# Kernel optimization log

Hardware: AMD Instinct MI355X
Metric: run time of the kernel (lower is better)

## Reference

```python
import jax, jax.numpy as jnp
import numpy as np
from jax import lax

NEG = -1e30  # finite stand-in for -inf to keep gradients clean
BLANK = 0


def _ctc_loss(log_probs, targets, logits_lengths, targets_lengths):
    # log_probs: (B, T, V) log-softmaxed; targets: (B, S) int; lengths: (B,)
    B, T, V = log_probs.shape
    S = targets.shape[1]
    L = 2 * S + 1  # extended label length: blank-interleaved

    # extended label sequence: [blank, t0, blank, t1, ..., blank]
    ext = jnp.zeros((B, L), dtype=targets.dtype).at[:, 1::2].set(targets)

    # gather log-probs of extended labels per time step -> (B, T, L)
    lp_ext = jnp.take_along_axis(
        log_probs, jnp.broadcast_to(ext[:, None, :], (B, T, L)), axis=2
    )

    # skip transition (s-2 -> s) allowed where ext[s] != blank and ext[s] != ext[s-2]
    skip = jnp.concatenate(
        [jnp.zeros((B, 2), dtype=bool),
         (ext[:, 2:] != ext[:, :-2]) & (ext[:, 2:] != BLANK)],
        axis=1,
    )

    # alpha init at t=0
    alpha0 = jnp.full((B, L), NEG, dtype=log_probs.dtype)
    alpha0 = alpha0.at[:, 0].set(lp_ext[:, 0, 0])
    alpha0 = alpha0.at[:, 1].set(
        jnp.where(targets_lengths > 0, lp_ext[:, 0, 1], NEG))

    neg1 = jnp.full((B, 1), NEG, dtype=log_probs.dtype)
    neg2 = jnp.full((B, 2), NEG, dtype=log_probs.dtype)

    def step(alpha, inp):
        lp_t, t = inp  # lp_t: (B, L)
        a1 = jnp.concatenate([neg1, alpha[:, :-1]], axis=1)
        a2 = jnp.where(skip, jnp.concatenate([neg2, alpha[:, :-2]], axis=1), NEG)
        new = jnp.logaddexp(jnp.logaddexp(alpha, a1), a2) + lp_t
        # freeze alpha once past each sequence's length so final read is at t=len-1
        alpha = jnp.where((t < logits_lengths)[:, None], new, alpha)
        return alpha, None

    lp_tbl = jnp.transpose(lp_ext, (1, 0, 2))  # (T, B, L)
    alpha, _ = lax.scan(step, alpha0, (lp_tbl[1:], jnp.arange(1, T)))

    # final states: last blank (index 2*tl) and last label (index 2*tl-1)
    idx_blank = (2 * targets_lengths).astype(jnp.int32)
    idx_label = jnp.maximum(2 * targets_lengths - 1, 0).astype(jnp.int32)
    a_blank = jnp.take_along_axis(alpha, idx_blank[:, None], axis=1)[:, 0]
    a_label = jnp.take_along_axis(alpha, idx_label[:, None], axis=1)[:, 0]
    a_label = jnp.where(targets_lengths > 0, a_label, NEG)
    return -jnp.logaddexp(a_blank, a_label)  # (B,)


def setup_inputs() -> dict:
    key = jax.random.key(0)
    k1, k2, k3, k4 = jax.random.split(key, 4)
    B, T, V, S = 32, 1024, 512, 128
    logits = jax.random.normal(k1, (B, T, V), dtype=jnp.float32)
    targets = jax.random.randint(k2, (B, S), 1, V, dtype=jnp.int32)  # avoid blank=0
    logits_lengths = jax.random.randint(k3, (B,), T // 2, T + 1, dtype=jnp.int32)
    targets_lengths = jax.random.randint(k4, (B,), S // 2, S + 1, dtype=jnp.int32)
    return {
        "logits": logits,
        "targets": targets,
        "logits_lengths": logits_lengths,
        "targets_lengths": targets_lengths,
    }


def reference(logits, targets, logits_lengths, targets_lengths):
    # after_logsoftmax=False -> apply log_softmax; time_major=False -> no permute
    log_probs = jax.nn.log_softmax(logits, axis=2)
    # reduce=None -> per-batch loss of shape (B,)
    return _ctc_loss(log_probs, targets, logits_lengths, targets_lengths)
```

## Files before the change

kernel.cpp:

```cpp
#include <hip/hip_runtime.h>

enum { B_ = 32, T_ = 1024, V_ = 512, S_ = 128 };

static constexpr float K2   = 1.4426950408889634f;
static constexpr float LN2F = 0.6931471805599453f;
#define BOOSTI 6

typedef float f32x4 __attribute__((ext_vector_type(4)));
#define AS1 __attribute__((address_space(1)))
#define AS3 __attribute__((address_space(3)))

#define DPPI(x, ctrl) __builtin_amdgcn_update_dpp(0, (x), (ctrl), 0xF, 0xF, true)
#define DPPF(x, ctrl) __int_as_float(DPPI(__float_as_int(x), (ctrl)))
#define DPP_WSR1(x) DPPF((x), 0x138)

__device__ __forceinline__ float dpp_wave_max_l63(float x) {
  x = fmaxf(x, DPPF(x, 0xB1));   x = fmaxf(x, DPPF(x, 0x4E));
  x = fmaxf(x, DPPF(x, 0x124));  x = fmaxf(x, DPPF(x, 0x128));
  x = fmaxf(x, DPPF(x, 0x142));  x = fmaxf(x, DPPF(x, 0x143));
  return x;
}

__global__ __launch_bounds__(256) void ctc_pre4(
    const float* __restrict__ logits, const int* __restrict__ targets,
    const int* __restrict__ tgtlen, f32x4* __restrict__ Q) {
  const int w = threadIdx.x >> 6, l = threadIdx.x & 63;
  const int row = blockIdx.x * 4 + w;
  const int b = row >> 10;
  const float* lrow = logits + (size_t)row * V_;
  const float4* r4 = (const float4*)lrow;
  float4 a = r4[l], c = r4[l + 64];
  float s = __builtin_exp2f(a.x * K2) + __builtin_exp2f(a.y * K2) +
            __builtin_exp2f(a.z * K2) + __builtin_exp2f(a.w * K2) +
            __builtin_exp2f(c.x * K2) + __builtin_exp2f(c.y * K2) +
            __builtin_exp2f(c.z * K2) + __builtin_exp2f(c.w * K2);
  #pragma unroll
  for (int off = 32; off; off >>= 1) s += __shfl_xor(s, off, 64);
  const float sh = (float)BOOSTI - __builtin_log2f(s);

  const int2 ee = ((const int2*)(targets + b * S_))[l];
  const int tl = tgtlen[b];
  const float lgb = __shfl(a.x, 0, 64);
  const float lg1 = lrow[ee.x];
  const float lg3 = lrow[ee.y];
  const float pb  = __builtin_exp2f(fmaf(lgb, K2, sh));
  const float pe1 = __builtin_exp2f(fmaf(lg1, K2, sh));
  const float pe3 = __builtin_exp2f(fmaf(lg3, K2, sh));
  const int smax = 2 * tl;
  f32x4 q;
  q.x = (4 * l + 1 <= smax) ? pe1 : 0.0f;
  q.y = (4 * l + 3 <= smax) ? pe3 : 0.0f;
  q.z = (4 * l     <= smax) ? pb  : 0.0f;
  q.w = (4 * l + 2 <= smax) ? pb  : 0.0f;
  Q[(size_t)row * 64 + l] = q;
}

__global__ __launch_bounds__(128, 1) void ctc_dp7(
    const f32x4* __restrict__ Q, const int* __restrict__ targets,
    const int* __restrict__ loglen, const int* __restrict__ tgtlen,
    float* __restrict__ out) {
  __shared__ f32x4 buf[2][32 * 64];
  __shared__ int flag_ready[2];
  __shared__ int flag_done[2];
  __shared__ float A[257];
  const int wv = threadIdx.x >> 6, l = threadIdx.x & 63;
  const int b = blockIdx.x;
  const int len = loglen[b], tl = tgtlen[b];
  const int nch = (len - 1 + 31) >> 5;
  const f32x4* Qb = Q + (size_t)b * T_ * 64;

  if (threadIdx.x == 0) {
    flag_ready[0] = 0; flag_ready[1] = 0;
    flag_done[0] = 0;  flag_done[1] = 0;
  }
  __syncthreads();

  if (wv == 1) {
    for (int c = 0; c < nch; ++c) {
      if (c >= 2) {
        while (((volatile int*)flag_done)[c & 1] < c - 1)
          __builtin_amdgcn_s_sleep(1);
      }
      const int r0 = 1 + 32 * c;
      #pragma unroll
      for (int i = 0; i < 32; ++i) {
        int row = r0 + i; if (row > T_ - 1) row = T_ - 1;
        __builtin_amdgcn_global_load_lds(
            (const AS1 void*)(const void*)(Qb + (size_t)row * 64 + l),
            (AS3 void*)(void*)(&buf[c & 1][i * 64]), 16, 0, 0);
      }
      asm volatile("s_waitcnt vmcnt(0)" ::: "memory");
      if (l == 0) ((volatile int*)flag_ready)[c & 1] = c + 1;
    }
    return;
  }

  const int2 ee = ((const int2*)(targets + b * S_))[l];
  const int e1 = ee.x, e3 = ee.y;
  const int em1 = __shfl_up(e3, 1);
  const float m1 = ((l > 0) && (e1 != 0) && (e1 != em1)) ? 1.0f : 0.0f;
  const float m3 = ((e3 != 0) && (e3 != e1)) ? 1.0f : 0.0f;
  const float v4l = ((l == 63) && (2 * tl >= 256)) ? 1.0f : 0.0f;

  f32x4 qi = Qb[l];
  float p0 = (l == 0) ? qi.z : 0.0f;
  float p1 = (l == 0) ? qi.x : 0.0f;
  float p2 = 0.0f, p3 = 0.0f, p4 = 0.0f;

  const unsigned bufbase = (unsigned)(uintptr_t)(AS3 char*)(void*)&buf[0][0];

  f32x4 q0, q1, q2, q3, q4, q5, q6, q7;
#define DSRO(R, O) asm volatile("ds_read_b128 %0, %1 offset:" #O \
      : "=&v"(R) : "v"(vb))
#define WTL(R, N) asm volatile("s_waitcnt lgkmcnt(" #N ")" : "+v"(R))

#define COMPUTE(RX) { \
    const float n1_  = DPP_WSR1(p3); \
    const float w0_ = (p0 + n1_) * RX.z; \
    const float w1_ = (p0 + p1 + n1_ * m1) * RX.x; \
    const float w2_ = (p1 + p2) * RX.w; \
    const float w3_ = (p2 + p3 + p1 * m3) * RX.y; \
    const float w4_ = (p4 + p3) * RX.w * v4l; \
    p0 = w0_; p1 = w1_; p2 = w2_; p3 = w3_; p4 = w4_; \
  }

#define RENORM { \
    float m_ = fmaxf(fmaxf(fmaxf(p0, p1), fmaxf(p2, p3)), p4); \
    m_ = dpp_wave_max_l63(m_); \
    const int wm_ = __builtin_amdgcn_readlane(__float_as_int(m_), 63); \
    const int e_ = (wm_ >> 23) & 0xFF; \
    const float sc_ = __int_as_float((254 - e_) << 23); \
    p0 *= sc_; p1 *= sc_; p2 *= sc_; p3 *= sc_; p4 *= sc_; \
    shift += e_ - 127; \
  }

#define FS(R, O)  { WTL(R, 7); COMPUTE(R); DSRO(R, O); }
#define FD(R, N)  { WTL(R, N); COMPUTE(R); }
#define TS(R, O, i)  { WTL(R, 7); if (t0 + (i) < len) COMPUTE(R); DSRO(R, O); }
#define TD(R, N, i)  { WTL(R, N); if (t0 + (i) < len) COMPUTE(R); }

  int shift = 0;
  for (int c = 0; c < nch; ++c) {
    const int t0 = 1 + 32 * c;
    while (((volatile int*)flag_ready)[c & 1] < c + 1)
      __builtin_amdgcn_s_sleep(1);
    const unsigned vb = bufbase + (unsigned)(c & 1) * 32768u + (unsigned)l * 16u;

    DSRO(q0, 0);    DSRO(q1, 1024); DSRO(q2, 2048); DSRO(q3, 3072);
    DSRO(q4, 4096); DSRO(q5, 5120); DSRO(q6, 6144); DSRO(q7, 7168);

    if (t0 + 31 < len) {
      FS(q0, 8192)  FS(q1, 9216)  FS(q2, 10240) FS(q3, 11264)
      FS(q4, 12288) FS(q5, 13312) FS(q6, 14336) FS(q7, 15360)
      FS(q0, 16384) FS(q1, 17408) FS(q2, 18432) FS(q3, 19456)
      FS(q4, 20480) FS(q5, 21504) FS(q6, 22528) FS(q7, 23552)
      RENORM
      FS(q0, 24576) FS(q1, 25600) FS(q2, 26624) FS(q3, 27648)
      FS(q4, 28672) FS(q5, 29696) FS(q6, 30720) FS(q7, 31744)
      FD(q0, 7) FD(q1, 6) FD(q2, 5) FD(q3, 4)
      FD(q4, 3) FD(q5, 2) FD(q6, 1) FD(q7, 0)
      RENORM
    } else {
      TS(q0, 8192, 0)   TS(q1, 9216, 1)   TS(q2, 10240, 2)  TS(q3, 11264, 3)
      TS(q4, 12288, 4)  TS(q5, 13312, 5)  TS(q6, 14336, 6)  TS(q7, 15360, 7)
      TS(q0, 16384, 8)  TS(q1, 17408, 9)  TS(q2, 18432, 10) TS(q3, 19456, 11)
      TS(q4, 20480, 12) TS(q5, 21504, 13) TS(q6, 22528, 14) TS(q7, 23552, 15)
      TS(q0, 24576, 16) TS(q1, 25600, 17) TS(q2, 26624, 18) TS(q3, 27648, 19)
      TS(q4, 28672, 20) TS(q5, 29696, 21) TS(q6, 30720, 22) TS(q7, 31744, 23)
      TD(q0, 7, 24) TD(q1, 6, 25) TD(q2, 5, 26) TD(q3, 4, 27)
      TD(q4, 3, 28) TD(q5, 2, 29) TD(q6, 1, 30) TD(q7, 0, 31)
    }

    asm volatile("s_waitcnt lgkmcnt(0)" ::: "memory");
    if (l == 0) ((volatile int*)flag_done)[c & 1] = c + 1;
  }

  A[4 * l + 0] = p0; A[4 * l + 1] = p1;
  A[4 * l + 2] = p2; A[4 * l + 3] = p3;
  if (l == 63) A[256] = p4;
  asm volatile("s_waitcnt lgkmcnt(0)" ::: "memory");
  if (l == 0) {
    const int ib = 2 * tl;
    const int il = (ib - 1) > 0 ? ib - 1 : 0;
    const float ab = A[ib];
    const float al = (tl > 0) ? A[il] : 0.0f;
    out[b] = -(__builtin_log2f(ab + al) + (float)(shift - BOOSTI * len)) * LN2F;
  }
}

extern "C" void kernel_launch(void* const* d_in, const int* in_sizes, int n_in,
                              void* d_out, int out_size, void* d_ws, size_t ws_size,
                              hipStream_t stream) {
  const float* logits  = (const float*)d_in[0];
  const int*   targets = (const int*)d_in[1];
  const int*   loglen  = (const int*)d_in[2];
  const int*   tgtlen  = (const int*)d_in[3];
  float* out = (float*)d_out;
  f32x4* Q = (f32x4*)d_ws;

  ctc_pre4<<<(B_ * T_) / 4, 256, 0, stream>>>(logits, targets, tgtlen, Q);
  ctc_dp7<<<B_, 128, 0, stream>>>(Q, targets, loglen, tgtlen, out);
}
```

Before: 66.35 us.

## Fuse log-softmax gather into DP kernel with three producer waves

Drops the separate preprocessing kernel and its workspace round-trip. Inside the single per-batch block, three producer wavefronts each compute the log-softmax normalisation and emission probabilities for every third 32-row chunk and write them to a triple-buffered LDS ring, while one consumer wave runs the alpha recursion. The consumer's LDS waits are also batched four reads at a time. The cost is that only 32 blocks now read the full logits tensor, so softmax throughput is bounded by three waves per CU and may not keep pace with the serial recursion.

Result: slower. 125.8 us (+89.6%).

```diff
diff --git a/kernel.cpp b/kernel.cpp
--- a/kernel.cpp
+++ b/kernel.cpp
@@ -7,7 +7,6 @@
 #define BOOSTI 6
 
 typedef float f32x4 __attribute__((ext_vector_type(4)));
-#define AS1 __attribute__((address_space(1)))
 #define AS3 __attribute__((address_space(3)))
 
 #define DPPI(x, ctrl) __builtin_amdgcn_update_dpp(0, (x), (ctrl), 0xF, 0xF, true)
@@ -20,102 +19,129 @@
   x = fmaxf(x, DPPF(x, 0x142));  x = fmaxf(x, DPPF(x, 0x143));
   return x;
 }
-
-__global__ __launch_bounds__(256) void ctc_pre4(
+#define DPP_SUM63(x) { \
+  x += DPPF(x, 0xB1);  x += DPPF(x, 0x4E);  x += DPPF(x, 0x124); \
+  x += DPPF(x, 0x128); x += DPPF(x, 0x142); x += DPPF(x, 0x143); }
+
+__global__ __launch_bounds__(256, 1) void ctc_fused(
     const float* __restrict__ logits, const int* __restrict__ targets,
-    const int* __restrict__ tgtlen, f32x4* __restrict__ Q) {
-  const int w = threadIdx.x >> 6, l = threadIdx.x & 63;
-  const int row = blockIdx.x * 4 + w;
-  const int b = row >> 10;
-  const float* lrow = logits + (size_t)row * V_;
-  const float4* r4 = (const float4*)lrow;
-  float4 a = r4[l], c = r4[l + 64];
-  float s = __builtin_exp2f(a.x * K2) + __builtin_exp2f(a.y * K2) +
-            __builtin_exp2f(a.z * K2) + __builtin_exp2f(a.w * K2) +
-            __builtin_exp2f(c.x * K2) + __builtin_exp2f(c.y * K2) +
-            __builtin_exp2f(c.z * K2) + __builtin_exp2f(c.w * K2);
-  #pragma unroll
-  for (int off = 32; off; off >>= 1) s += __shfl_xor(s, off, 64);
-  const float sh = (float)BOOSTI - __builtin_log2f(s);
-
-  const int2 ee = ((const int2*)(targets + b * S_))[l];
-  const int tl = tgtlen[b];
-  const float lgb = __shfl(a.x, 0, 64);
-  const float lg1 = lrow[ee.x];
-  const float lg3 = lrow[ee.y];
-  const float pb  = __builtin_exp2f(fmaf(lgb, K2, sh));
-  const float pe1 = __builtin_exp2f(fmaf(lg1, K2, sh));
-  const float pe3 = __builtin_exp2f(fmaf(lg3, K2, sh));
-  const int smax = 2 * tl;
-  f32x4 q;
-  q.x = (4 * l + 1 <= smax) ? pe1 : 0.0f;
-  q.y = (4 * l + 3 <= smax) ? pe3 : 0.0f;
-  q.z = (4 * l     <= smax) ? pb  : 0.0f;
-  q.w = (4 * l + 2 <= smax) ? pb  : 0.0f;
-  Q[(size_t)row * 64 + l] = q;
-}
-
-__global__ __launch_bounds__(128, 1) void ctc_dp7(
-    const f32x4* __restrict__ Q, const int* __restrict__ targets,
     const int* __restrict__ loglen, const int* __restrict__ tgtlen,
     float* __restrict__ out) {
-  __shared__ f32x4 buf[2][32 * 64];
-  __shared__ int flag_ready[2];
-  __shared__ int flag_done[2];
+  __shared__ f32x4 buf[3][32 * 64];
+  __shared__ int flag_ready[3], flag_done[3];
   __shared__ float A[257];
   const int wv = threadIdx.x >> 6, l = threadIdx.x & 63;
   const int b = blockIdx.x;
   const int len = loglen[b], tl = tgtlen[b];
   const int nch = (len - 1 + 31) >> 5;
-  const f32x4* Qb = Q + (size_t)b * T_ * 64;
+  const float* Lb = logits + (size_t)b * T_ * V_;
+
+  const int2 ee = ((const int2*)(targets + b * S_))[l];
+  const int e1 = ee.x, e3 = ee.y;
+  const int smax = 2 * tl;
 
   if (threadIdx.x == 0) {
-    flag_ready[0] = 0; flag_ready[1] = 0;
-    flag_done[0] = 0;  flag_done[1] = 0;
+    flag_ready[0] = flag_ready[1] = flag_ready[2] = 0;
+    flag_done[0] = flag_done[1] = flag_done[2] = 0;
   }
   __syncthreads();
 
-  if (wv == 1) {
-    for (int c = 0; c < nch; ++c) {
-      if (c >= 2) {
-        while (((volatile int*)flag_done)[c & 1] < c - 1)
+  if (wv != 0) {
+    const bool v0m = (4 * l     <= smax);
+    const bool v1m = (4 * l + 1 <= smax);
+    const bool v2m = (4 * l + 2 <= smax);
+    const bool v3m = (4 * l + 3 <= smax);
+    const int l16 = l * 16, e1b = e1 * 4, e3b = e3 * 4;
+
+    f32x4 pa0, pa1, pa2, pa3, pc0, pc1, pc2, pc3;
+    float g10, g11, g12, g13, g30, g31, g32, g33;
+
+#define PISS(s, ROW) { \
+    int rr_ = (ROW) > 1023 ? 1023 : (ROW); int rb_ = rr_ * 2048; \
+    asm volatile("global_load_dwordx4 %0, %1, %2" : "=&v"(pa##s) : "v"(rb_ + l16), "s"(Lb)); \
+    asm volatile("global_load_dwordx4 %0, %1, %2" : "=&v"(pc##s) : "v"(rb_ + 1024 + l16), "s"(Lb)); \
+    asm volatile("global_load_dword %0, %1, %2"   : "=&v"(g1##s) : "v"(rb_ + e1b), "s"(Lb)); \
+    asm volatile("global_load_dword %0, %1, %2"   : "=&v"(g3##s) : "v"(rb_ + e3b), "s"(Lb)); }
+
+#define PROW(i, s, VM, DO) { \
+    asm volatile("s_waitcnt vmcnt(" #VM ")" \
+        : "+v"(pa##s), "+v"(pc##s), "+v"(g1##s), "+v"(g3##s)); \
+    float x8_ = __builtin_exp2f(pa##s.x * K2) + __builtin_exp2f(pa##s.y * K2) + \
+                __builtin_exp2f(pa##s.z * K2) + __builtin_exp2f(pa##s.w * K2) + \
+                __builtin_exp2f(pc##s.x * K2) + __builtin_exp2f(pc##s.y * K2) + \
+                __builtin_exp2f(pc##s.z * K2) + __builtin_exp2f(pc##s.w * K2); \
+    DPP_SUM63(x8_); \
+    const float ss_ = __int_as_float(__builtin_amdgcn_readlane(__float_as_int(x8_), 63)); \
+    const float sh_ = (float)BOOSTI - __builtin_log2f(ss_); \
+    const float lgb_ = __int_as_float(__builtin_amdgcn_readfirstlane(__float_as_int(pa##s.x))); \
+    const float pe1_ = __builtin_exp2f(fmaf(g1##s, K2, sh_)); \
+    const float pe3_ = __builtin_exp2f(fmaf(g3##s, K2, sh_)); \
+    const float pb_  = __builtin_exp2f(fmaf(lgb_, K2, sh_)); \
+    f32x4 qq_; \
+    qq_.x = v1m ? pe1_ : 0.0f; qq_.y = v3m ? pe3_ : 0.0f; \
+    qq_.z = v0m ? pb_  : 0.0f; qq_.w = v2m ? pb_  : 0.0f; \
+    pbuf[(i) * 64 + l] = qq_; \
+    if (DO) { PISS(s, r0 + (i) + 4) } }
+
+#define PDRAIN asm volatile("s_waitcnt lgkmcnt(0)" ::: "memory");
+
+    for (int c = wv - 1; c < nch; c += 3) {
+      if (c >= 3) {
+        while (((volatile int*)flag_done)[c % 3] < c - 2)
           __builtin_amdgcn_s_sleep(1);
       }
       const int r0 = 1 + 32 * c;
-      #pragma unroll
-      for (int i = 0; i < 32; ++i) {
-        int row = r0 + i; if (row > T_ - 1) row = T_ - 1;
-        __builtin_amdgcn_global_load_lds(
-            (const AS1 void*)(const void*)(Qb + (size_t)row * 64 + l),
-            (AS3 void*)(void*)(&buf[c & 1][i * 64]), 16, 0, 0);
-      }
-      asm volatile("s_waitcnt vmcnt(0)" ::: "memory");
-      if (l == 0) ((volatile int*)flag_ready)[c & 1] = c + 1;
+      f32x4* pbuf = &buf[c % 3][0];
+      PISS(0, r0) PISS(1, r0 + 1) PISS(2, r0 + 2) PISS(3, r0 + 3)
+      PROW(0, 0, 12, 1)  PROW(1, 1, 12, 1)  PROW(2, 2, 12, 1)  PROW(3, 3, 12, 1)
+      PROW(4, 0, 12, 1)  PROW(5, 1, 12, 1)  PROW(6, 2, 12, 1)  PROW(7, 3, 12, 1)
+      PDRAIN
+      PROW(8, 0, 12, 1)  PROW(9, 1, 12, 1)  PROW(10, 2, 12, 1) PROW(11, 3, 12, 1)
+      PROW(12, 0, 12, 1) PROW(13, 1, 12, 1) PROW(14, 2, 12, 1) PROW(15, 3, 12, 1)
+      PDRAIN
+      PROW(16, 0, 12, 1) PROW(17, 1, 12, 1) PROW(18, 2, 12, 1) PROW(19, 3, 12, 1)
+      PROW(20, 0, 12, 1) PROW(21, 1, 12, 1) PROW(22, 2, 12, 1) PROW(23, 3, 12, 1)
+      PDRAIN
+      PROW(24, 0, 12, 1) PROW(25, 1, 12, 1) PROW(26, 2, 12, 1) PROW(27, 3, 12, 1)
+      PROW(28, 0, 12, 0) PROW(29, 1, 8, 0)  PROW(30, 2, 4, 0)  PROW(31, 3, 0, 0)
+      PDRAIN
+      if (l == 0) ((volatile int*)flag_ready)[c % 3] = c + 1;
     }
     return;
   }
 
-  const int2 ee = ((const int2*)(targets + b * S_))[l];
-  const int e1 = ee.x, e3 = ee.y;
   const int em1 = __shfl_up(e3, 1);
   const float m1 = ((l > 0) && (e1 != 0) && (e1 != em1)) ? 1.0f : 0.0f;
   const float m3 = ((e3 != 0) && (e3 != e1)) ? 1.0f : 0.0f;
-  const float v4l = ((l == 63) && (2 * tl >= 256)) ? 1.0f : 0.0f;
-
-  f32x4 qi = Qb[l];
-  float p0 = (l == 0) ? qi.z : 0.0f;
-  float p1 = (l == 0) ? qi.x : 0.0f;
+  const float v4l = ((l == 63) && (smax >= 256)) ? 1.0f : 0.0f;
+
+  const f32x4* R0 = (const f32x4*)Lb;
+  f32x4 a0 = R0[l], c0 = R0[l + 64];
+  float s0 = __builtin_exp2f(a0.x * K2) + __builtin_exp2f(a0.y * K2) +
+             __builtin_exp2f(a0.z * K2) + __builtin_exp2f(a0.w * K2) +
+             __builtin_exp2f(c0.x * K2) + __builtin_exp2f(c0.y * K2) +
+             __builtin_exp2f(c0.z * K2) + __builtin_exp2f(c0.w * K2);
+  DPP_SUM63(s0);
+  const float ss0 = __int_as_float(__builtin_amdgcn_readlane(__float_as_int(s0), 63));
+  const float sh0 = (float)BOOSTI - __builtin_log2f(ss0);
+  const float lgb0 = __int_as_float(__builtin_amdgcn_readfirstlane(__float_as_int(a0.x)));
+  const float lg10 = Lb[targets[b * S_]];
+  float p0 = (l == 0) ? __builtin_exp2f(fmaf(lgb0, K2, sh0)) : 0.0f;
+  float p1 = (l == 0) ? __builtin_exp2f(fmaf(lg10, K2, sh0)) : 0.0f;
   float p2 = 0.0f, p3 = 0.0f, p4 = 0.0f;
 
   const unsigned bufbase = (unsigned)(uintptr_t)(AS3 char*)(void*)&buf[0][0];
+  asm volatile("s_waitcnt vmcnt(0) lgkmcnt(0)" ::: "memory");
 
   f32x4 q0, q1, q2, q3, q4, q5, q6, q7;
 #define DSRO(R, O) asm volatile("ds_read_b128 %0, %1 offset:" #O \
-      : "=&v"(R) : "v"(vb))
-#define WTL(R, N) asm volatile("s_waitcnt lgkmcnt(" #N ")" : "+v"(R))
+      : "=&v"(R) : "v"(vb));
+#define WT4(RA, RB, RC, RD, N) asm volatile("s_waitcnt lgkmcnt(" #N ")" \
+      : "+v"(RA), "+v"(RB), "+v"(RC), "+v"(RD));
+#define WTL(R, N) asm volatile("s_waitcnt lgkmcnt(" #N ")" : "+v"(R));
 
 #define COMPUTE(RX) { \
-    const float n1_  = DPP_WSR1(p3); \
+    const float n1_ = DPP_WSR1(p3); \
     const float w0_ = (p0 + n1_) * RX.z; \
     const float w1_ = (p0 + p1 + n1_ * m1) * RX.x; \
     const float w2_ = (p1 + p2) * RX.w; \
@@ -123,7 +149,6 @@
     const float w4_ = (p4 + p3) * RX.w * v4l; \
     p0 = w0_; p1 = w1_; p2 = w2_; p3 = w3_; p4 = w4_; \
   }
-
 #define RENORM { \
     float m_ = fmaxf(fmaxf(fmaxf(p0, p1), fmaxf(p2, p3)), p4); \
     m_ = dpp_wave_max_l63(m_); \
@@ -133,32 +158,30 @@
     p0 *= sc_; p1 *= sc_; p2 *= sc_; p3 *= sc_; p4 *= sc_; \
     shift += e_ - 127; \
   }
-
-#define FS(R, O)  { WTL(R, 7); COMPUTE(R); DSRO(R, O); }
-#define FD(R, N)  { WTL(R, N); COMPUTE(R); }
-#define TS(R, O, i)  { WTL(R, 7); if (t0 + (i) < len) COMPUTE(R); DSRO(R, O); }
-#define TD(R, N, i)  { WTL(R, N); if (t0 + (i) < len) COMPUTE(R); }
+#define CD(R, O) { COMPUTE(R); DSRO(R, O); }
+#define TS(R, O, i) { WTL(R, 7); if (t0 + (i) < len) COMPUTE(R); DSRO(R, O); }
+#define TD(R, N, i) { WTL(R, N); if (t0 + (i) < len) COMPUTE(R); }
 
   int shift = 0;
   for (int c = 0; c < nch; ++c) {
     const int t0 = 1 + 32 * c;
-    while (((volatile int*)flag_ready)[c & 1] < c + 1)
+    while (((volatile int*)flag_ready)[c % 3] < c + 1)
       __builtin_amdgcn_s_sleep(1);
-    const unsigned vb = bufbase + (unsigned)(c & 1) * 32768u + (unsigned)l * 16u;
-
-    DSRO(q0, 0);    DSRO(q1, 1024); DSRO(q2, 2048); DSRO(q3, 3072);
-    DSRO(q4, 4096); DSRO(q5, 5120); DSRO(q6, 6144); DSRO(q7, 7168);
+    const unsigned vb = bufbase + (unsigned)(c % 3) * 32768u + (unsigned)l * 16u;
+
+    DSRO(q0, 0)    DSRO(q1, 1024) DSRO(q2, 2048) DSRO(q3, 3072)
+    DSRO(q4, 4096) DSRO(q5, 5120) DSRO(q6, 6144) DSRO(q7, 7168)
 
     if (t0 + 31 < len) {
-      FS(q0, 8192)  FS(q1, 9216)  FS(q2, 10240) FS(q3, 11264)
-      FS(q4, 12288) FS(q5, 13312) FS(q6, 14336) FS(q7, 15360)
-      FS(q0, 16384) FS(q1, 17408) FS(q2, 18432) FS(q3, 19456)
-      FS(q4, 20480) FS(q5, 21504) FS(q6, 22528) FS(q7, 23552)
+      WT4(q0, q1, q2, q3, 4) CD(q0, 8192)  CD(q1, 9216)  CD(q2, 10240) CD(q3, 11264)
+      WT4(q4, q5, q6, q7, 4) CD(q4, 12288) CD(q5, 13312) CD(q6, 14336) CD(q7, 15360)
+      WT4(q0, q1, q2, q3, 4) CD(q0, 16384) CD(q1, 17408) CD(q2, 18432) CD(q3, 19456)
+      WT4(q4, q5, q6, q7, 4) CD(q4, 20480) CD(q5, 21504) CD(q6, 22528) CD(q7, 23552)
       RENORM
-      FS(q0, 24576) FS(q1, 25600) FS(q2, 26624) FS(q3, 27648)
-      FS(q4, 28672) FS(q5, 29696) FS(q6, 30720) FS(q7, 31744)
-      FD(q0, 7) FD(q1, 6) FD(q2, 5) FD(q3, 4)
-      FD(q4, 3) FD(q5, 2) FD(q6, 1) FD(q7, 0)
+      WT4(q0, q1, q2, q3, 4) CD(q0, 24576) CD(q1, 25600) CD(q2, 26624) CD(q3, 27648)
+      WT4(q4, q5, q6, q7, 4) CD(q4, 28672) CD(q5, 29696) CD(q6, 30720) CD(q7, 31744)
+      WT4(q0, q1, q2, q3, 4) COMPUTE(q0) COMPUTE(q1) COMPUTE(q2) COMPUTE(q3)
+      WT4(q4, q5, q6, q7, 0) COMPUTE(q4) COMPUTE(q5) COMPUTE(q6) COMPUTE(q7)
       RENORM
     } else {
       TS(q0, 8192, 0)   TS(q1, 9216, 1)   TS(q2, 10240, 2)  TS(q3, 11264, 3)
@@ -172,7 +195,7 @@
     }
 
     asm volatile("s_waitcnt lgkmcnt(0)" ::: "memory");
-    if (l == 0) ((volatile int*)flag_done)[c & 1] = c + 1;
+    if (l == 0) ((volatile int*)flag_done)[c % 3] = c + 1;
   }
 
   A[4 * l + 0] = p0; A[4 * l + 1] = p1;
@@ -196,8 +219,5 @@
   const int*   loglen  = (const int*)d_in[2];
   const int*   tgtlen  = (const int*)d_in[3];
   float* out = (float*)d_out;
-  f32x4* Q = (f32x4*)d_ws;
-
-  ctc_pre4<<<(B_ * T_) / 4, 256, 0, stream>>>(logits, targets, tgtlen, Q);
-  ctc_dp7<<<B_, 128, 0, stream>>>(Q, targets, loglen, tgtlen, out);
+  ctc_fused<<<B_, 256, 0, stream>>>(logits, targets, loglen, tgtlen, out);
 }
```
